# Performance work log

Measured on AMD Instinct MI355X. Metric: run time of the kernel, lower is better.

## Reference

```python
import jax, jax.numpy as jnp
import numpy as np

EPS = 1e-8
RESOLUTION = 32
DILATION = 1


def _stencils(resolution=RESOLUTION, dilation=DILATION):
    # interior grid of resolution^2 samples in [-1, 1]^2 (cell centers)
    lin = (np.arange(resolution) + 0.5) / resolution * 2.0 - 1.0
    gy, gx = np.meshgrid(lin, lin, indexing='ij')
    inner = np.stack([gy.ravel(), gx.ravel()], -1).astype(np.float32)
    # perimeter ring dilated outward by `dilation` cells
    scale = (resolution + 2.0 * dilation) / resolution
    mask = np.zeros((resolution, resolution), bool)
    mask[0, :] = mask[-1, :] = mask[:, 0] = mask[:, -1] = True
    outer = (inner[mask.ravel()] * scale).astype(np.float32)
    # append homogeneous coordinate (matches torch.concat with ones)
    s_in = np.concatenate([inner, np.ones((inner.shape[0], 1), np.float32)], -1)
    s_out = np.concatenate([outer, np.ones((outer.shape[0], 1), np.float32)], -1)
    return jnp.asarray(s_in), jnp.asarray(s_out)


def _bilinear(image, pos):
    # image: (H, W); pos: (..., 2) pixel coords (row, col); clamped bilinear
    H, W = image.shape
    i = pos[..., 0]
    j = pos[..., 1]
    i0 = jnp.clip(jnp.floor(i), 0, H - 2).astype(jnp.int32)
    j0 = jnp.clip(jnp.floor(j), 0, W - 2).astype(jnp.int32)
    di = jnp.clip(i - i0, 0.0, 1.0)
    dj = jnp.clip(j - j0, 0.0, 1.0)
    v00 = image[i0, j0]
    v01 = image[i0, j0 + 1]
    v10 = image[i0 + 1, j0]
    v11 = image[i0 + 1, j0 + 1]
    return (v00 * (1 - di) * (1 - dj) + v01 * (1 - di) * dj
            + v10 * di * (1 - dj) + v11 * di * dj)


def setup_inputs() -> dict:
    key = jax.random.key(0)
    k1, k2 = jax.random.split(key)
    S, P = 4, 4096
    H = W = 2048
    u = jax.random.uniform(k1, (S, P, 5), dtype=jnp.float32)
    xy = u[..., :2] * (H - 1)              # centers inside the image
    ab = 4.0 + u[..., 2:4] * 20.0          # half extents in [4, 24] px
    th = u[..., 4:5] * jnp.float32(np.pi)  # angle in [0, pi)
    points = jnp.concatenate([xy, ab, th], axis=-1)
    points_mask = jnp.ones((S, P), dtype=jnp.float32)
    position_energy_map = jax.random.normal(k2, (1, H, W), dtype=jnp.float32)
    stencil_in, stencil_out = _stencils()
    return {"points": points, "points_mask": points_mask,
            "position_energy_map": position_energy_map,
            "stencil_in": stencil_in, "stencil_out": stencil_out}


def reference(points, points_mask, position_energy_map, stencil_in, stencil_out):
    # affine_from_state: (x, y, a, b, theta) -> 2x3 affine, shape (S, P, 2, 3)
    x, y = points[..., 0], points[..., 1]
    a, b = points[..., 2], points[..., 3]
    t = points[..., 4]
    c, s = jnp.cos(t), jnp.sin(t)
    A = jnp.stack([jnp.stack([a * c, -b * s, x], -1),
                   jnp.stack([a * s, b * c, y], -1)], -2)
    # stencil coordinates in image space: (S, P, n_stencil, 2)
    coords_in = jnp.einsum('spij,nj->spni', A, stencil_in)
    coords_out = jnp.einsum('spij,nj->spni', A, stencil_out)
    img = position_energy_map[0]
    in_values = _bilinear(img, coords_in)    # (S, P, n_in)
    out_values = _bilinear(img, coords_out)  # (S, P, n_out)
    # contrast_measure: t-test-like contrast along stencil dim
    m_in, m_out = in_values.mean(-1), out_values.mean(-1)
    v_in = in_values.var(-1, ddof=1)
    v_out = out_values.var(-1, ddof=1)
    contrast = (m_in - m_out) / jnp.sqrt(v_in + v_out + EPS)
    return contrast * points_mask
```

## Files before the change

kernel.cpp:

```cpp
#include <hip/hip_runtime.h>
#include <math.h>

__global__ __launch_bounds__(256) void contrast_kernel_fast(
    const float* __restrict__ points,
    const float* __restrict__ mask,
    const float* __restrict__ img,
    float* __restrict__ out,
    int n_points)
{
    constexpr int W = 2048;
    constexpr int H = 2048;
    constexpr float fImax = (float)(H - 2);
    constexpr float fJmax = (float)(W - 2);

    __shared__ float partial[4][4];

    const int wib  = (int)(threadIdx.x >> 6);
    const int lane = (int)(threadIdx.x & 63u);
    const int pid  = blockIdx.x * 2 + (wib >> 1);
    const int half = wib & 1;
    if (pid >= n_points) return;

    const float* pt = points + (size_t)pid * 5;
    const float px = pt[0];
    const float py = pt[1];
    const float a  = pt[2];
    const float b  = pt[3];
    const float th = pt[4];

    float sn, cs;
    sincosf(th, &sn, &cs);
    const float A00 = a * cs, A01 = -b * sn;
    const float A10 = a * sn, A11 =  b * cs;

    const int r8 = lane >> 3;
    const int c8 = lane & 7;
    const float sy0 = fmaf((float)r8, 0.0625f, 0.03125f) - 1.0f;
    const float sx0 = fmaf((float)c8, 0.0625f, 0.03125f) - 1.0f;
    const float ci0 = fmaf(A00, sy0, fmaf(A01, sx0, px));
    const float cj0 = fmaf(A10, sy0, fmaf(A11, sx0, py));
    const float A00h = A00 * 0.5f, A01h = A01 * 0.5f;
    const float A10h = A10 * 0.5f, A11h = A11 * 0.5f;

    float s0 = 0.f, q0 = 0.f, s1 = 0.f, q1 = 0.f;
    #pragma unroll
    for (int t = 0; t < 8; ++t) {
        const int tile = half * 8 + t;
        const float ftr = (float)(tile >> 2);
        const float ftc = (float)(tile & 3);
        const float ci = fmaf(A00h, ftr, fmaf(A01h, ftc, ci0));
        const float cj = fmaf(A10h, ftr, fmaf(A11h, ftc, cj0));
        const float fi = fminf(fmaxf(floorf(ci), 0.f), fImax);
        const float fj = fminf(fmaxf(floorf(cj), 0.f), fJmax);
        const float di = fminf(fmaxf(ci - fi, 0.f), 1.f);
        const float dj = fminf(fmaxf(cj - fj, 0.f), 1.f);
        const float* p0 = img + (((int)fi << 11) + (int)fj);
        float2 r0, r1;
        __builtin_memcpy(&r0, p0, sizeof(float2));
        __builtin_memcpy(&r1, p0 + W, sizeof(float2));
        const float top = fmaf(r0.y - r0.x, dj, r0.x);
        const float bot = fmaf(r1.y - r1.x, dj, r1.x);
        const float v   = fmaf(bot - top, di, top);
        if (t & 1) { s1 += v; q1 = fmaf(v, v, q1); }
        else       { s0 += v; q0 = fmaf(v, v, q0); }
    }
    float sum_in = s0 + s1;
    float sq_in  = q0 + q1;

    float sum_out = 0.f, sq_out = 0.f;
    {
        const int n = half * 62 + lane;
        if (lane < 62) {
            int row, col;
            if (n < 32)      { row = 0;                   col = n; }
            else if (n < 92) { row = 1 + ((n - 32) >> 1); col = (n & 1) * 31; }
            else             { row = 31;                  col = n - 92; }
            const float sy = (fmaf((float)row, 0.0625f, 0.03125f) - 1.0f) * 1.0625f;
            const float sx = (fmaf((float)col, 0.0625f, 0.03125f) - 1.0f) * 1.0625f;
            const float ci = fmaf(A00, sy, fmaf(A01, sx, px));
            const float cj = fmaf(A10, sy, fmaf(A11, sx, py));
            const float fi = fminf(fmaxf(floorf(ci), 0.f), fImax);
            const float fj = fminf(fmaxf(floorf(cj), 0.f), fJmax);
            const float di = fminf(fmaxf(ci - fi, 0.f), 1.f);
            const float dj = fminf(fmaxf(cj - fj, 0.f), 1.f);
            const float* p0 = img + (((int)fi << 11) + (int)fj);
            float2 r0, r1;
            __builtin_memcpy(&r0, p0, sizeof(float2));
            __builtin_memcpy(&r1, p0 + W, sizeof(float2));
            const float top = fmaf(r0.y - r0.x, dj, r0.x);
            const float bot = fmaf(r1.y - r1.x, dj, r1.x);
            const float v   = fmaf(bot - top, di, top);
            sum_out = v;
            sq_out  = v * v;
        }
    }

    #pragma unroll
    for (int off = 32; off > 0; off >>= 1) {
        sum_in  += __shfl_xor(sum_in,  off);
        sq_in   += __shfl_xor(sq_in,   off);
        sum_out += __shfl_xor(sum_out, off);
        sq_out  += __shfl_xor(sq_out,  off);
    }

    if (lane == 0) {
        partial[wib][0] = sum_in;
        partial[wib][1] = sq_in;
        partial[wib][2] = sum_out;
        partial[wib][3] = sq_out;
    }
    __syncthreads();

    if (lane == 0 && half == 0) {
        const float S_in  = partial[wib][0] + partial[wib + 1][0];
        const float Q_in  = partial[wib][1] + partial[wib + 1][1];
        const float S_out = partial[wib][2] + partial[wib + 1][2];
        const float Q_out = partial[wib][3] + partial[wib + 1][3];
        const float ni = 1024.f, no = 124.f;
        const float m_in  = S_in  / ni;
        const float m_out = S_out / no;
        const float v_in  = (Q_in  - ni * m_in  * m_in ) / (ni - 1.f);
        const float v_out = (Q_out - no * m_out * m_out) / (no - 1.f);
        const float contrast = (m_in - m_out) / sqrtf(v_in + v_out + 1e-8f);
        out[pid] = contrast * mask[pid];
    }
}

__global__ __launch_bounds__(256) void contrast_kernel_generic(
    const float* __restrict__ points, const float* __restrict__ mask,
    const float* __restrict__ img, const float* __restrict__ st_in,
    const float* __restrict__ st_out, float* __restrict__ out,
    int n_points, int n_in, int n_out, int Himg, int Wimg)
{
    const int wave = (int)((blockIdx.x * (unsigned)blockDim.x + threadIdx.x) >> 6);
    const int lane = (int)(threadIdx.x & 63u);
    if (wave >= n_points) return;
    const float* pt = points + (size_t)wave * 5;
    const float px = pt[0], py = pt[1], a = pt[2], b = pt[3], th = pt[4];
    float sn, cs; sincosf(th, &sn, &cs);
    const float A00 = a * cs, A01 = -b * sn, A10 = a * sn, A11 = b * cs;
    const float fImax = (float)(Himg - 2), fJmax = (float)(Wimg - 2);
    float sum_in = 0.f, sq_in = 0.f;
    for (int base = 0; base < n_in; base += 64) {
        const int n = base + lane;
        if (n < n_in) {
            const float sy = st_in[n * 3 + 0], sx = st_in[n * 3 + 1];
            const float ci = fmaf(A00, sy, fmaf(A01, sx, px));
            const float cj = fmaf(A10, sy, fmaf(A11, sx, py));
            const float fi = fminf(fmaxf(floorf(ci), 0.f), fImax);
            const float fj = fminf(fmaxf(floorf(cj), 0.f), fJmax);
            const float di = fminf(fmaxf(ci - fi, 0.f), 1.f);
            const float dj = fminf(fmaxf(cj - fj, 0.f), 1.f);
            const float* p0 = img + ((int)fi * Wimg + (int)fj);
            const float v00 = p0[0], v01 = p0[1], v10 = p0[Wimg], v11 = p0[Wimg + 1];
            const float top = fmaf(v01 - v00, dj, v00);
            const float bot = fmaf(v11 - v10, dj, v10);
            const float v = fmaf(bot - top, di, top);
            sum_in += v; sq_in = fmaf(v, v, sq_in);
        }
    }
    float sum_out = 0.f, sq_out = 0.f;
    for (int base = 0; base < n_out; base += 64) {
        const int n = base + lane;
        if (n < n_out) {
            const float sy = st_out[n * 3 + 0], sx = st_out[n * 3 + 1];
            const float ci = fmaf(A00, sy, fmaf(A01, sx, px));
            const float cj = fmaf(A10, sy, fmaf(A11, sx, py));
            const float fi = fminf(fmaxf(floorf(ci), 0.f), fImax);
            const float fj = fminf(fmaxf(floorf(cj), 0.f), fJmax);
            const float di = fminf(fmaxf(ci - fi, 0.f), 1.f);
            const float dj = fminf(fmaxf(cj - fj, 0.f), 1.f);
            const float* p0 = img + ((int)fi * Wimg + (int)fj);
            const float v00 = p0[0], v01 = p0[1], v10 = p0[Wimg], v11 = p0[Wimg + 1];
            const float top = fmaf(v01 - v00, dj, v00);
            const float bot = fmaf(v11 - v10, dj, v10);
            const float v = fmaf(bot - top, di, top);
            sum_out += v; sq_out = fmaf(v, v, sq_out);
        }
    }
    #pragma unroll
    for (int off = 32; off > 0; off >>= 1) {
        sum_in += __shfl_xor(sum_in, off);  sq_in += __shfl_xor(sq_in, off);
        sum_out += __shfl_xor(sum_out, off); sq_out += __shfl_xor(sq_out, off);
    }
    if (lane == 0) {
        const float ni = (float)n_in, no = (float)n_out;
        const float m_in = sum_in / ni, m_out = sum_out / no;
        const float v_in = (sq_in - ni * m_in * m_in) / (ni - 1.f);
        const float v_out = (sq_out - no * m_out * m_out) / (no - 1.f);
        const float contrast = (m_in - m_out) / sqrtf(v_in + v_out + 1e-8f);
        out[wave] = contrast * mask[wave];
    }
}

extern "C" void kernel_launch(void* const* d_in, const int* in_sizes, int n_in_bufs,
                              void* d_out, int out_size, void* d_ws, size_t ws_size,
                              hipStream_t stream) {
    (void)n_in_bufs; (void)d_ws; (void)ws_size; (void)out_size;
    const float* points = (const float*)d_in[0];
    const float* mask   = (const float*)d_in[1];
    const float* img    = (const float*)d_in[2];
    const float* st_in  = (const float*)d_in[3];
    const float* st_out = (const float*)d_in[4];
    float* out = (float*)d_out;

    const int n_points = in_sizes[0] / 5;
    const int n_in     = in_sizes[3] / 3;
    const int n_out    = in_sizes[4] / 3;
    const int hw       = in_sizes[2];

    if (n_in == 1024 && n_out == 124 && hw == 2048 * 2048) {
        const int blocks = (n_points + 1) / 2;
        contrast_kernel_fast<<<blocks, 256, 0, stream>>>(points, mask, img, out, n_points);
    } else {
        int Wimg = 1;
        while ((long long)Wimg * Wimg < (long long)hw) Wimg <<= 1;
        const int Himg = hw / Wimg;
        const int blocks = (n_points + 3) / 4;
        contrast_kernel_generic<<<blocks, 256, 0, stream>>>(points, mask, img, st_in, st_out,
                                                            out, n_points, n_in, n_out, Himg, Wimg);
    }
}
```

Baseline: 118.7 us.

## Convert image to fp16 in workspace and sample with an interior fast path

Adds a pre-pass that converts the 2048x2048 fp32 energy map to fp16 in the workspace, then runs a new contrast kernel that gathers bilinear taps from the half-size image. Each tap does two aligned 8-byte loads and extracts the needed pair with a shift. A bounding-box test per point picks a variant that skips the clamp logic when all stencil samples are inside the image. Halving the image footprint is meant to cut gather bandwidth and cache pressure, at the cost of an extra full-image conversion pass each call and reduced precision in the sampled values.

```diff
diff --git a/kernel.cpp b/kernel.cpp
--- a/kernel.cpp
+++ b/kernel.cpp
@@ -1,38 +1,57 @@
 #include <hip/hip_runtime.h>
+#include <hip/hip_fp16.h>
 #include <math.h>
 
-__global__ __launch_bounds__(256) void contrast_kernel_fast(
-    const float* __restrict__ points,
-    const float* __restrict__ mask,
-    const float* __restrict__ img,
-    float* __restrict__ out,
-    int n_points)
-{
-    constexpr int W = 2048;
-    constexpr int H = 2048;
-    constexpr float fImax = (float)(H - 2);
-    constexpr float fJmax = (float)(W - 2);
-
-    __shared__ float partial[4][4];
-
-    const int wib  = (int)(threadIdx.x >> 6);
-    const int lane = (int)(threadIdx.x & 63u);
-    const int pid  = blockIdx.x * 2 + (wib >> 1);
-    const int half = wib & 1;
-    if (pid >= n_points) return;
-
-    const float* pt = points + (size_t)pid * 5;
-    const float px = pt[0];
-    const float py = pt[1];
-    const float a  = pt[2];
-    const float b  = pt[3];
-    const float th = pt[4];
-
-    float sn, cs;
-    sincosf(th, &sn, &cs);
-    const float A00 = a * cs, A01 = -b * sn;
-    const float A10 = a * sn, A11 =  b * cs;
-
+
+__global__ __launch_bounds__(256) void convert_img_f16(
+    const float4* __restrict__ src, uint4* __restrict__ dst)
+{
+    const int t = blockIdx.x * 256 + (int)threadIdx.x;
+    const float4 a = src[(size_t)t * 2];
+    const float4 b = src[(size_t)t * 2 + 1];
+    union { __half2 h[4]; uint4 u; } o;
+    o.h[0] = __float22half2_rn(make_float2(a.x, a.y));
+    o.h[1] = __float22half2_rn(make_float2(a.z, a.w));
+    o.h[2] = __float22half2_rn(make_float2(b.x, b.y));
+    o.h[3] = __float22half2_rn(make_float2(b.z, b.w));
+    dst[t] = o.u;
+}
+
+template<bool CLAMP>
+__device__ __forceinline__ float tap16(const __half* __restrict__ img,
+                                       float ci, float cj)
+{
+    float fi = floorf(ci), fj = floorf(cj);
+    if (CLAMP) {
+        fi = fminf(fmaxf(fi, 0.f), 2046.f);
+        fj = fminf(fmaxf(fj, 0.f), 2046.f);
+    }
+    float di = ci - fi, dj = cj - fj;
+    if (CLAMP) {
+        di = fminf(fmaxf(di, 0.f), 1.f);
+        dj = fminf(fmaxf(dj, 0.f), 1.f);
+    }
+    const int base = ((int)fi << 11) + (int)fj;
+    const int even = base & ~1;
+    const int sh   = (base & 1) << 4;
+    uint2 q0, q1;
+    __builtin_memcpy(&q0, img + even, 8);
+    __builtin_memcpy(&q1, img + even + 2048, 8);
+    const unsigned p0 = (unsigned)((((unsigned long long)q0.y << 32) | q0.x) >> sh);
+    const unsigned p1 = (unsigned)((((unsigned long long)q1.y << 32) | q1.x) >> sh);
+    const float2 f0 = __half22float2(*reinterpret_cast<const __half2*>(&p0));
+    const float2 f1 = __half22float2(*reinterpret_cast<const __half2*>(&p1));
+    const float top = fmaf(f0.y - f0.x, dj, f0.x);
+    const float bot = fmaf(f1.y - f1.x, dj, f1.x);
+    return fmaf(bot - top, di, top);
+}
+
+template<bool CLAMP>
+__device__ __forceinline__ void accumulate16(
+    const __half* __restrict__ img, int lane, int half,
+    float A00, float A01, float A10, float A11, float px, float py,
+    float& sum_in, float& sq_in, float& sum_out, float& sq_out)
+{
     const int r8 = lane >> 3;
     const int c8 = lane & 7;
     const float sy0 = fmaf((float)r8, 0.0625f, 0.03125f) - 1.0f;
@@ -48,6 +67,132 @@
         const int tile = half * 8 + t;
         const float ftr = (float)(tile >> 2);
         const float ftc = (float)(tile & 3);
+        const float ci = fmaf(A00h, ftr, fmaf(A01h, ftc, ci0));
+        const float cj = fmaf(A10h, ftr, fmaf(A11h, ftc, cj0));
+        const float v = tap16<CLAMP>(img, ci, cj);
+        if (t & 1) { s1 += v; q1 = fmaf(v, v, q1); }
+        else       { s0 += v; q0 = fmaf(v, v, q0); }
+    }
+    sum_in = s0 + s1;
+    sq_in  = q0 + q1;
+
+    sum_out = 0.f; sq_out = 0.f;
+    const int n = half * 62 + lane;
+    if (lane < 62) {
+        int row, col;
+        if (n < 32)      { row = 0;                   col = n; }
+        else if (n < 92) { row = 1 + ((n - 32) >> 1); col = (n & 1) * 31; }
+        else             { row = 31;                  col = n - 92; }
+        const float sy = (fmaf((float)row, 0.0625f, 0.03125f) - 1.0f) * 1.0625f;
+        const float sx = (fmaf((float)col, 0.0625f, 0.03125f) - 1.0f) * 1.0625f;
+        const float ci = fmaf(A00, sy, fmaf(A01, sx, px));
+        const float cj = fmaf(A10, sy, fmaf(A11, sx, py));
+        const float v = tap16<CLAMP>(img, ci, cj);
+        sum_out = v;
+        sq_out  = v * v;
+    }
+}
+
+__global__ __launch_bounds__(256) void contrast_kernel_f16(
+    const float* __restrict__ points,
+    const float* __restrict__ mask,
+    const __half* __restrict__ img,
+    float* __restrict__ out,
+    int n_points)
+{
+    __shared__ float partial[4][4];
+
+    const int wib  = (int)(threadIdx.x >> 6);
+    const int lane = (int)(threadIdx.x & 63u);
+    const int pid  = blockIdx.x * 2 + (wib >> 1);
+    const int half = wib & 1;
+    if (pid >= n_points) return;
+
+    const float* pt = points + (size_t)pid * 5;
+    const float px = pt[0];
+    const float py = pt[1];
+    const float a  = pt[2];
+    const float b  = pt[3];
+    const float th = pt[4];
+
+    float sn, cs;
+    sincosf(th, &sn, &cs);
+    const float A00 = a * cs, A01 = -b * sn;
+    const float A10 = a * sn, A11 =  b * cs;
+
+    const float Ri = (fabsf(A00) + fabsf(A01)) * 1.04f;
+    const float Rj = (fabsf(A10) + fabsf(A11)) * 1.04f;
+    const bool interior = (px >= Ri + 0.5f) && (px <= 2046.0f - Ri) &&
+                          (py >= Rj + 0.5f) && (py <= 2046.0f - Rj);
+
+    float sum_in, sq_in, sum_out, sq_out;
+    if (interior) {
+        accumulate16<false>(img, lane, half, A00, A01, A10, A11, px, py,
+                            sum_in, sq_in, sum_out, sq_out);
+    } else {
+        accumulate16<true>(img, lane, half, A00, A01, A10, A11, px, py,
+                           sum_in, sq_in, sum_out, sq_out);
+    }
+
+    #pragma unroll
+    for (int off = 32; off > 0; off >>= 1) {
+        sum_in  += __shfl_xor(sum_in,  off);
+        sq_in   += __shfl_xor(sq_in,   off);
+        sum_out += __shfl_xor(sum_out, off);
+        sq_out  += __shfl_xor(sq_out,  off);
+    }
+
+    if (lane == 0) {
+        partial[wib][0] = sum_in;
+        partial[wib][1] = sq_in;
+        partial[wib][2] = sum_out;
+        partial[wib][3] = sq_out;
+    }
+    __syncthreads();
+
+    if (lane == 0 && half == 0) {
+        const float S_in  = partial[wib][0] + partial[wib + 1][0];
+        const float Q_in  = partial[wib][1] + partial[wib + 1][1];
+        const float S_out = partial[wib][2] + partial[wib + 1][2];
+        const float Q_out = partial[wib][3] + partial[wib + 1][3];
+        const float ni = 1024.f, no = 124.f;
+        const float m_in  = S_in  / ni;
+        const float m_out = S_out / no;
+        const float v_in  = (Q_in  - ni * m_in  * m_in ) / (ni - 1.f);
+        const float v_out = (Q_out - no * m_out * m_out) / (no - 1.f);
+        const float contrast = (m_in - m_out) / sqrtf(v_in + v_out + 1e-8f);
+        out[pid] = contrast * mask[pid];
+    }
+}
+
+__global__ __launch_bounds__(256) void contrast_kernel_fast(
+    const float* __restrict__ points, const float* __restrict__ mask,
+    const float* __restrict__ img, float* __restrict__ out, int n_points)
+{
+    constexpr int W = 2048;
+    constexpr float fImax = 2046.f, fJmax = 2046.f;
+    __shared__ float partial[4][4];
+    const int wib  = (int)(threadIdx.x >> 6);
+    const int lane = (int)(threadIdx.x & 63u);
+    const int pid  = blockIdx.x * 2 + (wib >> 1);
+    const int half = wib & 1;
+    if (pid >= n_points) return;
+    const float* pt = points + (size_t)pid * 5;
+    const float px = pt[0], py = pt[1], a = pt[2], b = pt[3], th = pt[4];
+    float sn, cs; sincosf(th, &sn, &cs);
+    const float A00 = a * cs, A01 = -b * sn, A10 = a * sn, A11 = b * cs;
+    const int r8 = lane >> 3, c8 = lane & 7;
+    const float sy0 = fmaf((float)r8, 0.0625f, 0.03125f) - 1.0f;
+    const float sx0 = fmaf((float)c8, 0.0625f, 0.03125f) - 1.0f;
+    const float ci0 = fmaf(A00, sy0, fmaf(A01, sx0, px));
+    const float cj0 = fmaf(A10, sy0, fmaf(A11, sx0, py));
+    const float A00h = A00 * 0.5f, A01h = A01 * 0.5f;
+    const float A10h = A10 * 0.5f, A11h = A11 * 0.5f;
+    float s0 = 0.f, q0 = 0.f, s1 = 0.f, q1 = 0.f;
+    #pragma unroll
+    for (int t = 0; t < 8; ++t) {
+        const int tile = half * 8 + t;
+        const float ftr = (float)(tile >> 2), ftc = (float)(tile & 3);
         const float ci = fmaf(A00h, ftr, fmaf(A01h, ftc, ci0));
         const float cj = fmaf(A10h, ftr, fmaf(A11h, ftc, cj0));
         const float fi = fminf(fmaxf(floorf(ci), 0.f), fImax);
@@ -60,41 +205,35 @@
         __builtin_memcpy(&r1, p0 + W, sizeof(float2));
         const float top = fmaf(r0.y - r0.x, dj, r0.x);
         const float bot = fmaf(r1.y - r1.x, dj, r1.x);
-        const float v   = fmaf(bot - top, di, top);
+        const float v = fmaf(bot - top, di, top);
         if (t & 1) { s1 += v; q1 = fmaf(v, v, q1); }
         else       { s0 += v; q0 = fmaf(v, v, q0); }
     }
-    float sum_in = s0 + s1;
-    float sq_in  = q0 + q1;
-
+    float sum_in = s0 + s1, sq_in = q0 + q1;
     float sum_out = 0.f, sq_out = 0.f;
-    {
-        const int n = half * 62 + lane;
-        if (lane < 62) {
-            int row, col;
-            if (n < 32)      { row = 0;                   col = n; }
-            else if (n < 92) { row = 1 + ((n - 32) >> 1); col = (n & 1) * 31; }
-            else             { row = 31;                  col = n - 92; }
-            const float sy = (fmaf((float)row, 0.0625f, 0.03125f) - 1.0f) * 1.0625f;
-            const float sx = (fmaf((float)col, 0.0625f, 0.03125f) - 1.0f) * 1.0625f;
-            const float ci = fmaf(A00, sy, fmaf(A01, sx, px));
-            const float cj = fmaf(A10, sy, fmaf(A11, sx, py));
-            const float fi = fminf(fmaxf(floorf(ci), 0.f), fImax);
-            const float fj = fminf(fmaxf(floorf(cj), 0.f), fJmax);
-            const float di = fminf(fmaxf(ci - fi, 0.f), 1.f);
-            const float dj = fminf(fmaxf(cj - fj, 0.f), 1.f);
-            const float* p0 = img + (((int)fi << 11) + (int)fj);
-            float2 r0, r1;
-            __builtin_memcpy(&r0, p0, sizeof(float2));
-            __builtin_memcpy(&r1, p0 + W, sizeof(float2));
-            const float top = fmaf(r0.y - r0.x, dj, r0.x);
-            const float bot = fmaf(r1.y - r1.x, dj, r1.x);
-            const float v   = fmaf(bot - top, di, top);
-            sum_out = v;
-            sq_out  = v * v;
-        }
-    }
-
+    const int n = half * 62 + lane;
+    if (lane < 62) {
+        int row, col;
+        if (n < 32)      { row = 0;                   col = n; }
+        else if (n < 92) { row = 1 + ((n - 32) >> 1); col = (n & 1) * 31; }
+        else             { row = 31;                  col = n - 92; }
+        const float sy = (fmaf((float)row, 0.0625f, 0.03125f) - 1.0f) * 1.0625f;
+        const float sx = (fmaf((float)col, 0.0625f, 0.03125f) - 1.0f) * 1.0625f;
+        const float ci = fmaf(A00, sy, fmaf(A01, sx, px));
+        const float cj = fmaf(A10, sy, fmaf(A11, sx, py));
+        const float fi = fminf(fmaxf(floorf(ci), 0.f), fImax);
+        const float fj = fminf(fmaxf(floorf(cj), 0.f), fJmax);
+        const float di = fminf(fmaxf(ci - fi, 0.f), 1.f);
+        const float dj = fminf(fmaxf(cj - fj, 0.f), 1.f);
+        const float* p0 = img + (((int)fi << 11) + (int)fj);
+        float2 r0, r1;
+        __builtin_memcpy(&r0, p0, sizeof(float2));
+        __builtin_memcpy(&r1, p0 + W, sizeof(float2));
+        const float top = fmaf(r0.y - r0.x, dj, r0.x);
+        const float bot = fmaf(r1.y - r1.x, dj, r1.x);
+        const float v = fmaf(bot - top, di, top);
+        sum_out = v; sq_out = v * v;
+    }
     #pragma unroll
     for (int off = 32; off > 0; off >>= 1) {
         sum_in  += __shfl_xor(sum_in,  off);
@@ -102,23 +241,18 @@
         sum_out += __shfl_xor(sum_out, off);
         sq_out  += __shfl_xor(sq_out,  off);
     }
-
     if (lane == 0) {
-        partial[wib][0] = sum_in;
-        partial[wib][1] = sq_in;
-        partial[wib][2] = sum_out;
-        partial[wib][3] = sq_out;
+        partial[wib][0] = sum_in; partial[wib][1] = sq_in;
+        partial[wib][2] = sum_out; partial[wib][3] = sq_out;
     }
     __syncthreads();
-
     if (lane == 0 && half == 0) {
-        const float S_in  = partial[wib][0] + partial[wib + 1][0];
-        const float Q_in  = partial[wib][1] + partial[wib + 1][1];
+        const float S_in = partial[wib][0] + partial[wib + 1][0];
+        const float Q_in = partial[wib][1] + partial[wib + 1][1];
         const float S_out = partial[wib][2] + partial[wib + 1][2];
         const float Q_out = partial[wib][3] + partial[wib + 1][3];
         const float ni = 1024.f, no = 124.f;
-        const float m_in  = S_in  / ni;
-        const float m_out = S_out / no;
+        const float m_in = S_in / ni, m_out = S_out / no;
         const float v_in  = (Q_in  - ni * m_in  * m_in ) / (ni - 1.f);
         const float v_out = (Q_out - no * m_out * m_out) / (no - 1.f);
         const float contrast = (m_in - m_out) / sqrtf(v_in + v_out + 1e-8f);
@@ -196,7 +330,7 @@
 extern "C" void kernel_launch(void* const* d_in, const int* in_sizes, int n_in_bufs,
                               void* d_out, int out_size, void* d_ws, size_t ws_size,
                               hipStream_t stream) {
-    (void)n_in_bufs; (void)d_ws; (void)ws_size; (void)out_size;
+    (void)n_in_bufs; (void)out_size;
     const float* points = (const float*)d_in[0];
     const float* mask   = (const float*)d_in[1];
     const float* img    = (const float*)d_in[2];
@@ -209,7 +343,15 @@
     const int n_out    = in_sizes[4] / 3;
     const int hw       = in_sizes[2];
 
-    if (n_in == 1024 && n_out == 124 && hw == 2048 * 2048) {
+    const bool canonical = (n_in == 1024 && n_out == 124 && hw == 2048 * 2048);
+    const size_t f16_bytes = (size_t)hw * sizeof(__half) + 256;
+
+    if (canonical && ws_size >= f16_bytes) {
+        __half* img16 = (__half*)d_ws;
+        convert_img_f16<<<hw / (256 * 8), 256, 0, stream>>>((const float4*)img, (uint4*)img16);
+        const int blocks = (n_points + 1) / 2;
+        contrast_kernel_f16<<<blocks, 256, 0, stream>>>(points, mask, img16, out, n_points);
+    } else if (canonical) {
         const int blocks = (n_points + 1) / 2;
         contrast_kernel_fast<<<blocks, 256, 0, stream>>>(points, mask, img, out, n_points);
     } else {
```

Result: no change. 121.1 us (+2.0%).
